# Optimization experiments

Measured on AMD Instinct MI355X. Metric: run time of the kernel, lower is better.

## Reference

```python
import jax, jax.numpy as jnp
import numpy as np

CHUNK = 64  # _HYMBA_SCAN_CHUNK default
HEAD_DIM = 128
STATE_DIM = 128


def setup_inputs() -> dict:
    key = jax.random.key(0)
    ks = jax.random.split(key, 6)
    B, T = 8, 8192
    x = jax.random.normal(ks[0], (B, T, HEAD_DIM), dtype=jnp.float32)
    log_A = jax.random.normal(ks[1], (STATE_DIM,), dtype=jnp.float32) * 0.5
    # torch Linear weights are (out_features, in_features); kaiming-uniform-ish init
    lim = 1.0 / np.sqrt(HEAD_DIM)
    W_B = jax.random.uniform(ks[2], (STATE_DIM, HEAD_DIM), jnp.float32, -lim, lim)
    W_C = jax.random.uniform(ks[3], (STATE_DIM, HEAD_DIM), jnp.float32, -lim, lim)
    W_dt = jax.random.uniform(ks[4], (STATE_DIM, HEAD_DIM), jnp.float32, -lim, lim)
    b_dt = jnp.full((STATE_DIM,), -4.0, dtype=jnp.float32)
    lim_o = 1.0 / np.sqrt(STATE_DIM)
    W_out = jax.random.uniform(ks[5], (HEAD_DIM, STATE_DIM), jnp.float32, -lim_o, lim_o)
    return {"x": x, "log_A": log_A, "W_B": W_B, "W_C": W_C,
            "W_dt": W_dt, "b_dt": b_dt, "W_out": W_out}


def _scan_chunks(log_a, u, chunk_size=CHUNK):
    # log_a, u: (B, T, S) fp32; exact chunk-parallel diagonal recurrence
    B, T, S = u.shape
    nc = T // chunk_size
    la = log_a.reshape(B, nc, chunk_size, S).transpose(1, 0, 2, 3)  # (nc,B,ck,S)
    uu = u.reshape(B, nc, chunk_size, S).transpose(1, 0, 2, 3)

    def step(h0, inp):
        la_c, u_c = inp                                   # (B, ck, S)
        log_p = jnp.clip(jnp.cumsum(la_c, axis=1), -30.0, 0.0)
        p = jnp.exp(log_p)
        h = p * jnp.cumsum(u_c * jnp.exp(-log_p), axis=1) + p * h0[:, None, :]
        return h[:, -1, :], h

    h0 = jnp.zeros((B, S), dtype=jnp.float32)
    _, h_chunks = jax.lax.scan(step, h0, (la, uu))        # (nc, B, ck, S)
    return h_chunks.transpose(1, 0, 2, 3).reshape(B, T, S)


def reference(x, log_A, W_B, W_C, W_dt, b_dt, W_out):
    xf = x.astype(jnp.float32)
    dt = jnp.minimum(jax.nn.softplus(jnp.einsum('btd,sd->bts', xf, W_dt) + b_dt), 1.0)
    A = -jnp.minimum(jnp.exp(log_A.astype(jnp.float32)), 10.0)   # (S,)
    log_a = jnp.clip(dt * A[None, None, :], -0.5, 0.0)
    Bx = jnp.einsum('btd,sd->bts', xf, W_B) * dt
    C = jnp.einsum('btd,sd->bts', xf, W_C)
    h = _scan_chunks(log_a, Bx)                                   # (B,T,S)
    y = jnp.sum(C * h, axis=-1, keepdims=True)                    # (B,T,1)
    out = jnp.einsum('bts,ds->btd', h.astype(x.dtype), W_out)
    return out + y.astype(x.dtype) * x[..., :1]
```

## Files before the change

### kernel.cpp

```cpp
#include <hip/hip_runtime.h>
#include <hip/hip_bf16.h>

#define B_ 8
#define T_ 8192
#define D_ 128
#define S_ 128
#define CK 64
#define NC 128
#define NCHUNK (B_*NC)

typedef __attribute__((ext_vector_type(8))) __bf16 bf16x8;
typedef __attribute__((ext_vector_type(4))) float floatx4;

#define WS_WBF     0
#define WS_AVEC    32768
#define WS_PART    32896

__device__ __forceinline__ unsigned short f2bf(float f) {
  __hip_bfloat16 b = __float2bfloat16(f);
  return *(unsigned short*)&b;
}

__device__ __forceinline__ float softplus1(float z) {
  float sp = fmaxf(z, 0.0f) + __logf(1.0f + __expf(-fabsf(z)));
  return fminf(sp, 1.0f);
}

__device__ __forceinline__ unsigned long long part_load(const unsigned long long* p) {
  return __hip_atomic_load(p, __ATOMIC_RELAXED, __HIP_MEMORY_SCOPE_AGENT);
}
__device__ __forceinline__ void part_store(unsigned long long* p, unsigned long long v) {
  __hip_atomic_store(p, v, __ATOMIC_RELAXED, __HIP_MEMORY_SCOPE_AGENT);
}

__global__ __launch_bounds__(256) void k0_prep(
    const float* __restrict__ Wdt, const float* __restrict__ WB,
    const float* __restrict__ WC,  const float* __restrict__ Wout,
    const float* __restrict__ logA, float* __restrict__ ws) {
  unsigned short* wb = (unsigned short*)(ws + WS_WBF);
  const float* srcs[4] = {Wdt, WB, WC, Wout};
  int gid = blockIdx.x * 256 + threadIdx.x;
  if (gid < 8192) {
    int fid = gid;
    int lane = fid & 63;
    int kk   = (fid >> 6) & 3;
    int nt   = (fid >> 8) & 7;
    int m    = fid >> 11;
    int c = lane & 15, g = lane >> 4;
    const float* src = srcs[m] + (16 * nt + c) * 128 + 32 * kk + 8 * g;
    float4 v0 = *(const float4*)src;
    float4 v1 = *(const float4*)(src + 4);
    unsigned short o[8];
    o[0] = f2bf(v0.x); o[1] = f2bf(v0.y); o[2] = f2bf(v0.z); o[3] = f2bf(v0.w);
    o[4] = f2bf(v1.x); o[5] = f2bf(v1.y); o[6] = f2bf(v1.z); o[7] = f2bf(v1.w);
    *(ushort4*)&wb[fid * 8]     = *(ushort4*)&o[0];
    *(ushort4*)&wb[fid * 8 + 4] = *(ushort4*)&o[4];
  }
  unsigned long long* part = (unsigned long long*)(ws + WS_PART);
#pragma unroll
  for (int i = 0; i < 8; ++i)
    part[gid + 16384 * i] = 0ull;
  if (blockIdx.x == 0 && threadIdx.x < 128)
    ws[WS_AVEC + threadIdx.x] = -fminf(expf(logA[threadIdx.x]), 10.0f);
}

#define WFRAG(mat, nt, kk) \
  (*(const bf16x8*)&wb[(((((mat) * 8 + (nt)) * 4) + (kk)) * 64 + lane) * 8])

__global__ __launch_bounds__(256, 4) void k_main(
    const float* __restrict__ x, const float* __restrict__ bdt,
    float* __restrict__ out, float* __restrict__ ws) {
  __shared__ __align__(16) unsigned short xb[64 * 136];
  __shared__ float x0s[64];
  __shared__ float yxa[4 * 64];

  const int tid  = threadIdx.x;
  const int bc   = blockIdx.x;
  const int b    = bc & 7;
  const int cidx = bc >> 3;
  const long chunk_t0 = (long)b * T_ + (long)cidx * CK;
  const int w    = tid >> 6;
  const int lane = tid & 63;
  const int g    = lane >> 4;
  const int c    = lane & 15;

  float Av2[2], Bd2[2];
#pragma unroll
  for (int ntl = 0; ntl < 2; ++ntl) {
    int s = 32 * w + 16 * ntl + c;
    Av2[ntl] = ws[WS_AVEC + s];
    Bd2[ntl] = bdt[s];
  }

  const float4* x4 = (const float4*)(x + chunk_t0 * D_);
#pragma unroll
  for (int i = 0; i < 8; ++i) {
    int f4 = tid + 256 * i;
    int t  = f4 >> 5;
    int d0 = (f4 & 31) << 2;
    float4 v = x4[f4];
    ushort4 o;
    o.x = f2bf(v.x); o.y = f2bf(v.y); o.z = f2bf(v.z); o.w = f2bf(v.w);
    *(ushort4*)&xb[t * 136 + d0] = o;
  }
  if (tid < 64) x0s[tid] = x[(chunk_t0 + tid) * D_];
  __syncthreads();

  const unsigned short* wb = (const unsigned short*)(ws + WS_WBF);
  unsigned long long* part = (unsigned long long*)(ws + WS_PART);

  floatx4 A_[2][4], U_[2][4];
#pragma unroll
  for (int ntl = 0; ntl < 2; ++ntl)
#pragma unroll
    for (int mt = 0; mt < 4; ++mt) {
      A_[ntl][mt] = (floatx4){0.f, 0.f, 0.f, 0.f};
      U_[ntl][mt] = (floatx4){0.f, 0.f, 0.f, 0.f};
    }
#pragma unroll
  for (int kk = 0; kk < 4; ++kk) {
    bf16x8 fD0 = WFRAG(0, 2 * w + 0, kk);
    bf16x8 fD1 = WFRAG(0, 2 * w + 1, kk);
    bf16x8 fB0 = WFRAG(1, 2 * w + 0, kk);
    bf16x8 fB1 = WFRAG(1, 2 * w + 1, kk);
#pragma unroll
    for (int mt = 0; mt < 4; ++mt) {
      bf16x8 a = *(const bf16x8*)&xb[(16 * mt + c) * 136 + 8 * g + 32 * kk];
      A_[0][mt] = __builtin_amdgcn_mfma_f32_16x16x32_bf16(a, fD0, A_[0][mt], 0, 0, 0);
      A_[1][mt] = __builtin_amdgcn_mfma_f32_16x16x32_bf16(a, fD1, A_[1][mt], 0, 0, 0);
      U_[0][mt] = __builtin_amdgcn_mfma_f32_16x16x32_bf16(a, fB0, U_[0][mt], 0, 0, 0);
      U_[1][mt] = __builtin_amdgcn_mfma_f32_16x16x32_bf16(a, fB1, U_[1][mt], 0, 0, 0);
    }
  }

#pragma unroll
  for (int ntl = 0; ntl < 2; ++ntl)
#pragma unroll
    for (int mt = 0; mt < 4; ++mt)
#pragma unroll
      for (int i = 0; i < 4; ++i) {
        float dt = softplus1(A_[ntl][mt][i] + Bd2[ntl]);
        float u  = U_[ntl][mt][i] * dt;
        float la = fmaxf(fminf(dt * Av2[ntl], 0.0f), -0.5f);
        A_[ntl][mt][i] = __expf(la);
        U_[ntl][mt][i] = u;
      }

  float PcT[2], HcT[2];
#pragma unroll
  for (int ntl = 0; ntl < 2; ++ntl) {
    float Pc = 1.0f, Hc = 0.0f;
#pragma unroll
    for (int mt = 0; mt < 4; ++mt) {
      float P = A_[ntl][mt][0], H = U_[ntl][mt][0];
#pragma unroll
      for (int i = 1; i < 4; ++i) {
        H = fmaf(H, A_[ntl][mt][i], U_[ntl][mt][i]);
        P = P * A_[ntl][mt][i];
        A_[ntl][mt][i] = P;
        U_[ntl][mt][i] = H;
      }
      float Po = __shfl(P, (lane - 16) & 63), Ho = __shfl(H, (lane - 16) & 63);
      if (g >= 1) { H = fmaf(Ho, P, H); P = Po * P; }
      Po = __shfl(P, (lane - 32) & 63); Ho = __shfl(H, (lane - 32) & 63);
      if (g >= 2) { H = fmaf(Ho, P, H); P = Po * P; }
      float Pt = __shfl(P, 48 + c);
      float Ht = __shfl(H, 48 + c);
      float Pe = __shfl(P, (lane - 16) & 63), He = __shfl(H, (lane - 16) & 63);
      if (g == 0) { Pe = 1.0f; He = 0.0f; }
      float Hent = fmaf(Pe, Hc, He);
      float Pent = Pe * Pc;
#pragma unroll
      for (int i = 0; i < 4; ++i) {
        U_[ntl][mt][i] = fmaf(A_[ntl][mt][i], Hent, U_[ntl][mt][i]);
        A_[ntl][mt][i] = A_[ntl][mt][i] * Pent;
      }
      Hc = fmaf(Pt, Hc, Ht);
      Pc = Pc * Pt;
    }
    PcT[ntl] = Pc; HcT[ntl] = Hc;
  }

  if (g == 0) {
#pragma unroll
    for (int ntl = 0; ntl < 2; ++ntl) {
      unsigned long long v = ((unsigned long long)__float_as_uint(HcT[ntl]) << 32) |
                             (unsigned long long)__float_as_uint(PcT[ntl]);
      part_store(&part[bc * 128 + 32 * w + 16 * ntl + c], v);
    }
  }

  floatx4 Cc[2][4];
#pragma unroll
  for (int ntl = 0; ntl < 2; ++ntl)
#pragma unroll
    for (int mt = 0; mt < 4; ++mt) Cc[ntl][mt] = (floatx4){0.f, 0.f, 0.f, 0.f};
#pragma unroll
  for (int kk = 0; kk < 4; ++kk) {
    bf16x8 fC0 = WFRAG(2, 2 * w + 0, kk);
    bf16x8 fC1 = WFRAG(2, 2 * w + 1, kk);
#pragma unroll
    for (int mt = 0; mt < 4; ++mt) {
      bf16x8 a = *(const bf16x8*)&xb[(16 * mt + c) * 136 + 8 * g + 32 * kk];
      Cc[0][mt] = __builtin_amdgcn_mfma_f32_16x16x32_bf16(a, fC0, Cc[0][mt], 0, 0, 0);
      Cc[1][mt] = __builtin_amdgcn_mfma_f32_16x16x32_bf16(a, fC1, Cc[1][mt], 0, 0, 0);
    }
  }

  float h0v[2];
  {
    const int s    = 32 * w + (lane & 31);
    const int half = lane >> 5;
    float RP = 1.0f, RH = 0.0f;
    const int K   = (cidx + 1) >> 1;
    int j         = half ? (cidx - K - 1) : (cidx - 1);
    const int jlo = half ? 0 : (cidx - K);
    while (j >= jlo) {
      int nb = j - jlo + 1; if (nb > 8) nb = 8;
      unsigned long long v[8];
#pragma unroll
      for (int q = 0; q < 8; ++q)
        if (q < nb) v[q] = part_load(&part[(((j - q) << 3) | b) * 128 + s]);
#pragma unroll
      for (int q = 0; q < 8; ++q) {
        if (q < nb) {
          unsigned long long vv = v[q];
          const unsigned long long* ap = &part[(((j - q) << 3) | b) * 128 + s];
          while ((unsigned)vv == 0u) {
            __builtin_amdgcn_s_sleep(2);
            vv = part_load(ap);
          }
          float Pj = __uint_as_float((unsigned)vv);
          float Hj = __uint_as_float((unsigned)(vv >> 32));
          RH = fmaf(RP, Hj, RH);
          RP = RP * Pj;
        }
      }
      j -= nb;
    }
    float oP = __shfl_xor(RP, 32), oH = __shfl_xor(RH, 32);
    float Pn = half ? oP : RP, Hn = half ? oH : RH;
    float Hf = half ? RH : oH;
    float H0 = fmaf(Pn, Hf, Hn);
#pragma unroll
    for (int ntl = 0; ntl < 2; ++ntl)
      h0v[ntl] = __shfl(H0, 16 * ntl + c);
  }

  __syncthreads();

  float yv[4][4];
#pragma unroll
  for (int mt = 0; mt < 4; ++mt)
#pragma unroll
    for (int i = 0; i < 4; ++i) yv[mt][i] = 0.0f;
#pragma unroll
  for (int ntl = 0; ntl < 2; ++ntl)
#pragma unroll
    for (int mt = 0; mt < 4; ++mt)
#pragma unroll
      for (int i = 0; i < 4; ++i) {
        float hv = fmaf(A_[ntl][mt][i], h0v[ntl], U_[ntl][mt][i]);
        yv[mt][i] = fmaf(Cc[ntl][mt][i], hv, yv[mt][i]);
        xb[(16 * mt + 4 * g + i) * 136 + 32 * w + 16 * ntl + c] = f2bf(hv);
      }
#pragma unroll
  for (int mt = 0; mt < 4; ++mt)
#pragma unroll
    for (int i = 0; i < 4; ++i) {
      float y = yv[mt][i];
      y += __shfl_xor(y, 1);
      y += __shfl_xor(y, 2);
      y += __shfl_xor(y, 4);
      y += __shfl_xor(y, 8);
      if (c == 0) yxa[w * 64 + 16 * mt + 4 * g + i] = y;
    }

  __syncthreads();
  if (tid < 64) {
    float y = yxa[tid] + yxa[64 + tid] + yxa[128 + tid] + yxa[192 + tid];
    x0s[tid] = y * x0s[tid];
  }
  __syncthreads();

  floatx4 Oc[2][4];
#pragma unroll
  for (int ntl = 0; ntl < 2; ++ntl)
#pragma unroll
    for (int mt = 0; mt < 4; ++mt) Oc[ntl][mt] = (floatx4){0.f, 0.f, 0.f, 0.f};
#pragma unroll
  for (int kk = 0; kk < 4; ++kk) {
    bf16x8 fO0 = WFRAG(3, 2 * w + 0, kk);
    bf16x8 fO1 = WFRAG(3, 2 * w + 1, kk);
#pragma unroll
    for (int mt = 0; mt < 4; ++mt) {
      bf16x8 h = *(const bf16x8*)&xb[(16 * mt + c) * 136 + 8 * g + 32 * kk];
      Oc[0][mt] = __builtin_amdgcn_mfma_f32_16x16x32_bf16(h, fO0, Oc[0][mt], 0, 0, 0);
      Oc[1][mt] = __builtin_amdgcn_mfma_f32_16x16x32_bf16(h, fO1, Oc[1][mt], 0, 0, 0);
    }
  }

#pragma unroll
  for (int mt = 0; mt < 4; ++mt)
#pragma unroll
    for (int i = 0; i < 4; ++i) {
      int row = 16 * mt + 4 * g + i;
      float yt = x0s[row];
#pragma unroll
      for (int ntl = 0; ntl < 2; ++ntl)
        out[(chunk_t0 + row) * D_ + 32 * w + 16 * ntl + c] = Oc[ntl][mt][i] + yt;
    }
}

extern "C" void kernel_launch(void* const* d_in, const int* in_sizes, int n_in,
                              void* d_out, int out_size, void* d_ws, size_t ws_size,
                              hipStream_t stream) {
  const float* x    = (const float*)d_in[0];
  const float* logA = (const float*)d_in[1];
  const float* W_B  = (const float*)d_in[2];
  const float* W_C  = (const float*)d_in[3];
  const float* W_dt = (const float*)d_in[4];
  const float* b_dt = (const float*)d_in[5];
  const float* W_out= (const float*)d_in[6];
  float* out = (float*)d_out;
  float* ws  = (float*)d_ws;

  k0_prep<<<64, 256, 0, stream>>>(W_dt, W_B, W_C, W_out, logA, ws);
  k_main<<<NCHUNK, 256, 0, stream>>>(x, b_dt, out, ws);
}
```

Measured before the change: 124.1 us.

## Add decoupled look-back with inclusive prefixes for cross-chunk state propagation

Each chunk block now publishes an inclusive prefix (P,H) after computing its starting state, alongside its local aggregate. Successor blocks walk backward and stop as soon as they find an inclusive prefix, replacing the previous split-half full reduction over all predecessor aggregates. The aim is to cut the look-back from linear in chunk index to a short walk, at the cost of a second workspace region and extra stores. The change also pads the LDS row stride from 136 to 140 and lowers launch bounds occupancy from 4 to 3.

```diff
diff --git a/kernel.cpp b/kernel.cpp
--- a/kernel.cpp
+++ b/kernel.cpp
@@ -8,6 +8,7 @@
 #define CK 64
 #define NC 128
 #define NCHUNK (B_*NC)
+#define XSTR 140
 
 typedef __attribute__((ext_vector_type(8))) __bf16 bf16x8;
 typedef __attribute__((ext_vector_type(4))) float floatx4;
@@ -15,6 +16,7 @@
 #define WS_WBF     0
 #define WS_AVEC    32768
 #define WS_PART    32896
+#define WS_PARTI   (32896 + 262144)
 
 __device__ __forceinline__ unsigned short f2bf(float f) {
   __hip_bfloat16 b = __float2bfloat16(f);
@@ -58,7 +60,7 @@
   }
   unsigned long long* part = (unsigned long long*)(ws + WS_PART);
 #pragma unroll
-  for (int i = 0; i < 8; ++i)
+  for (int i = 0; i < 16; ++i)
     part[gid + 16384 * i] = 0ull;
   if (blockIdx.x == 0 && threadIdx.x < 128)
     ws[WS_AVEC + threadIdx.x] = -fminf(expf(logA[threadIdx.x]), 10.0f);
@@ -67,10 +69,10 @@
 #define WFRAG(mat, nt, kk) \
   (*(const bf16x8*)&wb[(((((mat) * 8 + (nt)) * 4) + (kk)) * 64 + lane) * 8])
 
-__global__ __launch_bounds__(256, 4) void k_main(
+__global__ __launch_bounds__(256, 3) void k_main(
     const float* __restrict__ x, const float* __restrict__ bdt,
     float* __restrict__ out, float* __restrict__ ws) {
-  __shared__ __align__(16) unsigned short xb[64 * 136];
+  __shared__ __align__(16) unsigned short xb[64 * XSTR];
   __shared__ float x0s[64];
   __shared__ float yxa[4 * 64];
 
@@ -101,13 +103,14 @@
     float4 v = x4[f4];
     ushort4 o;
     o.x = f2bf(v.x); o.y = f2bf(v.y); o.z = f2bf(v.z); o.w = f2bf(v.w);
-    *(ushort4*)&xb[t * 136 + d0] = o;
+    *(ushort4*)&xb[t * XSTR + d0] = o;
   }
   if (tid < 64) x0s[tid] = x[(chunk_t0 + tid) * D_];
   __syncthreads();
 
   const unsigned short* wb = (const unsigned short*)(ws + WS_WBF);
-  unsigned long long* part = (unsigned long long*)(ws + WS_PART);
+  unsigned long long* partA = (unsigned long long*)(ws + WS_PART);
+  unsigned long long* partI = (unsigned long long*)(ws + WS_PARTI);
 
   floatx4 A_[2][4], U_[2][4];
 #pragma unroll
@@ -125,7 +128,7 @@
     bf16x8 fB1 = WFRAG(1, 2 * w + 1, kk);
 #pragma unroll
     for (int mt = 0; mt < 4; ++mt) {
-      bf16x8 a = *(const bf16x8*)&xb[(16 * mt + c) * 136 + 8 * g + 32 * kk];
+      bf16x8 a = *(const bf16x8*)&xb[(16 * mt + c) * XSTR + 8 * g + 32 * kk];
       A_[0][mt] = __builtin_amdgcn_mfma_f32_16x16x32_bf16(a, fD0, A_[0][mt], 0, 0, 0);
       A_[1][mt] = __builtin_amdgcn_mfma_f32_16x16x32_bf16(a, fD1, A_[1][mt], 0, 0, 0);
       U_[0][mt] = __builtin_amdgcn_mfma_f32_16x16x32_bf16(a, fB0, U_[0][mt], 0, 0, 0);
@@ -186,7 +189,7 @@
     for (int ntl = 0; ntl < 2; ++ntl) {
       unsigned long long v = ((unsigned long long)__float_as_uint(HcT[ntl]) << 32) |
                              (unsigned long long)__float_as_uint(PcT[ntl]);
-      part_store(&part[bc * 128 + 32 * w + 16 * ntl + c], v);
+      part_store(&partA[bc * 128 + 32 * w + 16 * ntl + c], v);
     }
   }
 
@@ -201,50 +204,65 @@
     bf16x8 fC1 = WFRAG(2, 2 * w + 1, kk);
 #pragma unroll
     for (int mt = 0; mt < 4; ++mt) {
-      bf16x8 a = *(const bf16x8*)&xb[(16 * mt + c) * 136 + 8 * g + 32 * kk];
+      bf16x8 a = *(const bf16x8*)&xb[(16 * mt + c) * XSTR + 8 * g + 32 * kk];
       Cc[0][mt] = __builtin_amdgcn_mfma_f32_16x16x32_bf16(a, fC0, Cc[0][mt], 0, 0, 0);
       Cc[1][mt] = __builtin_amdgcn_mfma_f32_16x16x32_bf16(a, fC1, Cc[1][mt], 0, 0, 0);
     }
   }
 
   float h0v[2];
+  float P0f = 1.0f, H0f = 0.0f;
   {
-    const int s    = 32 * w + (lane & 31);
-    const int half = lane >> 5;
-    float RP = 1.0f, RH = 0.0f;
-    const int K   = (cidx + 1) >> 1;
-    int j         = half ? (cidx - K - 1) : (cidx - 1);
-    const int jlo = half ? 0 : (cidx - K);
-    while (j >= jlo) {
-      int nb = j - jlo + 1; if (nb > 8) nb = 8;
-      unsigned long long v[8];
-#pragma unroll
-      for (int q = 0; q < 8; ++q)
-        if (q < nb) v[q] = part_load(&part[(((j - q) << 3) | b) * 128 + s]);
-#pragma unroll
-      for (int q = 0; q < 8; ++q) {
-        if (q < nb) {
-          unsigned long long vv = v[q];
-          const unsigned long long* ap = &part[(((j - q) << 3) | b) * 128 + s];
-          while ((unsigned)vv == 0u) {
-            __builtin_amdgcn_s_sleep(2);
-            vv = part_load(ap);
+    const int s = 32 * w + (lane & 31);
+    if (lane < 32) {
+      float RP = 1.0f, RH = 0.0f;
+      int j = cidx - 1;
+      while (j >= 0) {
+        unsigned long long vi = part_load(&partI[((j << 3) | b) * 128 + s]);
+        if ((unsigned)vi != 0u) {
+          float Pi = __uint_as_float((unsigned)vi);
+          float Hi = __uint_as_float((unsigned)(vi >> 32));
+          RH = fmaf(RP, Hi, RH);
+          RP = RP * Pi;
+          break;
+        }
+        int nb = (j >= 7) ? 8 : (j + 1);
+        unsigned long long v[8];
+#pragma unroll
+        for (int q = 0; q < 8; ++q)
+          if (q < nb) v[q] = part_load(&partA[(((j - q) << 3) | b) * 128 + s]);
+#pragma unroll
+        for (int q = 0; q < 8; ++q) {
+          if (q < nb) {
+            unsigned long long vv = v[q];
+            const unsigned long long* ap = &partA[(((j - q) << 3) | b) * 128 + s];
+            while ((unsigned)vv == 0u) {
+              __builtin_amdgcn_s_sleep(2);
+              vv = part_load(ap);
+            }
+            float Pj = __uint_as_float((unsigned)vv);
+            float Hj = __uint_as_float((unsigned)(vv >> 32));
+            RH = fmaf(RP, Hj, RH);
+            RP = RP * Pj;
           }
-          float Pj = __uint_as_float((unsigned)vv);
-          float Hj = __uint_as_float((unsigned)(vv >> 32));
-          RH = fmaf(RP, Hj, RH);
-          RP = RP * Pj;
         }
-      }
-      j -= nb;
-    }
-    float oP = __shfl_xor(RP, 32), oH = __shfl_xor(RH, 32);
-    float Pn = half ? oP : RP, Hn = half ? oH : RH;
-    float Hf = half ? RH : oH;
-    float H0 = fmaf(Pn, Hf, Hn);
+        j -= nb;
+      }
+      P0f = RP; H0f = RH;
+    }
 #pragma unroll
     for (int ntl = 0; ntl < 2; ++ntl)
-      h0v[ntl] = __shfl(H0, 16 * ntl + c);
+      h0v[ntl] = __shfl(H0f, 16 * ntl + c);
+  }
+
+  if (lane < 32) {
+    float Pct = (lane & 16) ? PcT[1] : PcT[0];
+    float Hct = (lane & 16) ? HcT[1] : HcT[0];
+    float Pinc = fmaxf(Pct * P0f, 1.2e-38f);
+    float Hinc = fmaf(Pct, H0f, Hct);
+    unsigned long long vI = ((unsigned long long)__float_as_uint(Hinc) << 32) |
+                            (unsigned long long)__float_as_uint(Pinc);
+    part_store(&partI[bc * 128 + 32 * w + lane], vI);
   }
 
   __syncthreads();
@@ -262,7 +280,7 @@
       for (int i = 0; i < 4; ++i) {
         float hv = fmaf(A_[ntl][mt][i], h0v[ntl], U_[ntl][mt][i]);
         yv[mt][i] = fmaf(Cc[ntl][mt][i], hv, yv[mt][i]);
-        xb[(16 * mt + 4 * g + i) * 136 + 32 * w + 16 * ntl + c] = f2bf(hv);
+        xb[(16 * mt + 4 * g + i) * XSTR + 32 * w + 16 * ntl + c] = f2bf(hv);
       }
 #pragma unroll
   for (int mt = 0; mt < 4; ++mt)
@@ -294,7 +312,7 @@
     bf16x8 fO1 = WFRAG(3, 2 * w + 1, kk);
 #pragma unroll
     for (int mt = 0; mt < 4; ++mt) {
-      bf16x8 h = *(const bf16x8*)&xb[(16 * mt + c) * 136 + 8 * g + 32 * kk];
+      bf16x8 h = *(const bf16x8*)&xb[(16 * mt + c) * XSTR + 8 * g + 32 * kk];
       Oc[0][mt] = __builtin_amdgcn_mfma_f32_16x16x32_bf16(h, fO0, Oc[0][mt], 0, 0, 0);
       Oc[1][mt] = __builtin_amdgcn_mfma_f32_16x16x32_bf16(h, fO1, Oc[1][mt], 0, 0, 0);
     }
```

Result: faster. 117.7 us (-5.2%).
